# Kernel tuning notes

Measured on AMD Instinct MI355X. Metric: run time of the kernel, lower is better.

Reference implementation:

```python
import jax, jax.numpy as jnp
import numpy as np


def _phi(z, conv_w, conv_b):
    # z: (H, W, S, 1) -> 3x3 SAME conv over state channels -> softmax over states
    x = jnp.transpose(z[..., 0], (2, 0, 1))[None]  # (1, S, H, W)
    y = jax.lax.conv_general_dilated(
        x, conv_w, window_strides=(1, 1), padding='SAME',
        dimension_numbers=('NCHW', 'OIHW', 'NCHW')) + conv_b[None, :, None, None]
    return jax.nn.softmax(jnp.transpose(y[0], (1, 2, 0)), axis=2)[..., None]  # (H, W, S, 1)


def _update(obs, P, u_k, w_k_O, conv_w, conv_b):
    H, W, O = obs.shape
    S = P.shape[0]
    # b = P^T @ obs per cell: b[h,w,s] = sum_o P[o,s] * obs[h,w,o]
    b = jnp.einsum('os,hwo->hws', P, obs)[..., None]  # (H, W, S, 1)
    # Analytic Jacobian db/dP: deriv_b[h,w,s,0,i,j] = obs[h,w,i] * delta(s==j)
    eye = jnp.eye(S, O, dtype=obs.dtype)
    deriv_b = (obs[:, :, None, :, None] * eye[None, None, :, None, :])[:, :, :, None, :, :]  # (H,W,S,1,S,O)

    Bu = b * u_k                                  # (H, W, S, 1)
    bu = jnp.sum(Bu, axis=2, keepdims=True)       # (H, W, 1, 1)
    Z = Bu / bu                                   # Bu / bu

    u_kp1 = _phi(Z, conv_w, conv_b)               # (H, W, S, 1)

    # Sensitivity recursion for obs params (quotient rule on Bu/bu)
    du = deriv_b * u_k[..., None, None] + b[..., None, None] * w_k_O  # (H,W,S,1,S,O)
    term1 = du * bu[..., None, None]
    term2 = jnp.expand_dims(jnp.sum(du, axis=2), 3) * Bu[..., None, None]
    w_pre = (term1 - term2) / bu[..., None, None] ** 2                # (H,W,S,1,S,O)

    # J @ w  ==  9 JVPs of Phi at Z with tangent columns of w (exact, avoids dense (HWS)^2 Jacobian)
    tangents = jnp.moveaxis(w_pre.reshape(H, W, S, 1, S * O), -1, 0)  # (S*O, H, W, S, 1)
    jvp1 = lambda t: jax.jvp(lambda z: _phi(z, conv_w, conv_b), (Z,), (t,))[1]
    w_kp1_O = jnp.moveaxis(jax.vmap(jvp1)(tangents), 0, -1).reshape(H, W, S, 1, S, O)
    return u_kp1, w_kp1_O


def setup_inputs() -> dict:
    key = jax.random.key(0)
    k1, k2, k3 = jax.random.split(key, 3)
    H = W = 512
    S = O = 3
    obs = jax.random.uniform(k1, (H, W, O), dtype=jnp.float32)
    obs_param_matrix = jnp.ones((S, O), jnp.float32) / O          # row-stochastic init
    u_k = jnp.ones((H, W, S, 1), jnp.float32) / S                 # uniform belief
    w_k_O = jnp.zeros((H, W, S, 1, S, O), jnp.float32)
    conv_w = jax.random.normal(k2, (S, S, 3, 3), jnp.float32) * 0.1
    conv_b = jax.random.normal(k3, (S,), jnp.float32) * 0.1
    return {'obs': obs, 'obs_param_matrix': obs_param_matrix, 'u_k': u_k,
            'w_k_O': w_k_O, 'conv_w': conv_w, 'conv_b': conv_b}


def reference(obs, obs_param_matrix, u_k, w_k_O, conv_w, conv_b):
    return _update(obs, obs_param_matrix, u_k, w_k_O, conv_w, conv_b)
```

## Files before the change

kernel.cpp:

```cpp
#include <hip/hip_runtime.h>

#define IMH 512
#define IMW 512
#define TW 16
#define TH 8
#define HW_ (TW + 2)
#define HH_ (TH + 2)
#define NHALO (HW_ * HH_)
#define NPIX (TW * TH)
#define ROW 31

typedef float f4 __attribute__((ext_vector_type(4)));
typedef float f4a __attribute__((ext_vector_type(4), aligned(4)));
typedef float f2a __attribute__((ext_vector_type(2), aligned(4)));

__global__ __launch_bounds__(256, 4)
void hmm_fused(const float* __restrict__ obs,
               const float* __restrict__ P,
               const float* __restrict__ u_k,
               const float* __restrict__ w_k,
               const float* __restrict__ conv_w,
               const float* __restrict__ conv_b,
               float* __restrict__ out) {
    __shared__ __align__(16) float lds[NHALO * ROW];
    __shared__ f4 p_aux4[NPIX];

    const int tid = threadIdx.x;
    const int w0 = blockIdx.x * TW;
    const int h0 = blockIdx.y * TH;

    float Pm[9];
#pragma unroll
    for (int i = 0; i < 9; ++i) Pm[i] = P[i];

    if (tid < NHALO) {
        const int p = tid;
        const int hh = h0 + p / HW_ - 1;
        const int ww = w0 + p % HW_ - 1;
        float* row = &lds[p * ROW];
        if (hh < 0 || hh >= IMH || ww < 0 || ww >= IMW) {
#pragma unroll
            for (int c = 0; c < 30; ++c) row[c] = 0.0f;
        } else {
            const int pix = hh * IMW + ww;

            const f2a o01 = *(const f2a*)(obs + pix * 3);
            const float o2 = obs[pix * 3 + 2];
            const f2a u01 = *(const f2a*)(u_k + pix * 3);
            const float u2 = u_k[pix * 3 + 2];
            const float ov[3] = {o01.x, o01.y, o2};
            const float us[3] = {u01.x, u01.y, u2};

            const float* wkp = &w_k[(size_t)pix * 27];
            float wreg[27];
            {
                const f4a* v4 = (const f4a*)wkp;
                const f4a a0 = v4[0], a1 = v4[1], a2 = v4[2], a3 = v4[3], a4 = v4[4], a5 = v4[5];
                const f2a a6 = *(const f2a*)(wkp + 24);
                const float a7 = wkp[26];
                wreg[0] = a0.x;  wreg[1] = a0.y;  wreg[2] = a0.z;  wreg[3] = a0.w;
                wreg[4] = a1.x;  wreg[5] = a1.y;  wreg[6] = a1.z;  wreg[7] = a1.w;
                wreg[8] = a2.x;  wreg[9] = a2.y;  wreg[10] = a2.z; wreg[11] = a2.w;
                wreg[12] = a3.x; wreg[13] = a3.y; wreg[14] = a3.z; wreg[15] = a3.w;
                wreg[16] = a4.x; wreg[17] = a4.y; wreg[18] = a4.z; wreg[19] = a4.w;
                wreg[20] = a5.x; wreg[21] = a5.y; wreg[22] = a5.z; wreg[23] = a5.w;
                wreg[24] = a6.x; wreg[25] = a6.y; wreg[26] = a7;
            }

            float b[3], Bu[3], bu = 0.0f;
#pragma unroll
            for (int s = 0; s < 3; ++s) {
                b[s] = Pm[0 * 3 + s] * ov[0] + Pm[1 * 3 + s] * ov[1] + Pm[2 * 3 + s] * ov[2];
                Bu[s] = b[s] * us[s];
                bu += Bu[s];
            }
            const float inv_bu = 1.0f / bu;
            float Z[3];
#pragma unroll
            for (int s = 0; s < 3; ++s) { Z[s] = Bu[s] * inv_bu; row[s] = Z[s]; }

#pragma unroll
            for (int i = 0; i < 3; ++i) {
#pragma unroll
                for (int j = 0; j < 3; ++j) {
                    const int ij = i * 3 + j;
                    float du[3], sdu = 0.0f;
#pragma unroll
                    for (int s = 0; s < 3; ++s) {
                        float d = b[s] * wreg[s * 9 + ij];
                        if (s == j) d += ov[i] * us[s];
                        du[s] = d;
                        sdu += d;
                    }
#pragma unroll
                    for (int s = 0; s < 3; ++s)
                        row[(1 + ij) * 3 + s] = (du[s] - sdu * Z[s]) * inv_bu;
                }
            }
        }
    }

    float cw[81];
#pragma unroll
    for (int i = 0; i < 81; ++i) cw[i] = conv_w[i];
    const float cb0 = conv_b[0], cb1 = conv_b[1], cb2 = conv_b[2];

    __syncthreads();

    float* outw = out + IMH * IMW * 3;

    if (tid < NPIX) {
        const int tx = tid & 15, ty = tid >> 4;
        const int hp = (ty + 1) * HW_ + (tx + 1);
        const int pix = (h0 + ty) * IMW + (w0 + tx);
        float y0 = cb0, y1 = cb1, y2 = cb2;
#pragma unroll
        for (int ky = 0; ky < 3; ++ky) {
#pragma unroll
            for (int kx = 0; kx < 3; ++kx) {
                const float* nb = &lds[(hp + (ky - 1) * HW_ + (kx - 1)) * ROW];
                const float v0 = nb[0], v1 = nb[1], v2 = nb[2];
                const int T = ky * 3 + kx;
                y0 += cw[0 + T] * v0 + cw[9 + T] * v1 + cw[18 + T] * v2;
                y1 += cw[27 + T] * v0 + cw[36 + T] * v1 + cw[45 + T] * v2;
                y2 += cw[54 + T] * v0 + cw[63 + T] * v1 + cw[72 + T] * v2;
            }
        }
        const float m = fmaxf(y0, fmaxf(y1, y2));
        const float e0 = __expf(y0 - m), e1 = __expf(y1 - m), e2 = __expf(y2 - m);
        const float inv = 1.0f / (e0 + e1 + e2);
        const float p0 = e0 * inv, p1 = e1 * inv, p2 = e2 * inv;
        out[pix * 3 + 0] = p0; out[pix * 3 + 1] = p1; out[pix * 3 + 2] = p2;
        p_aux4[tid] = (f4){p0, p1, p2, 0.0f};
    }

    __syncthreads();

    if (tid < 144) {
        const int x = tid & 15;
        const int g = (tid >> 4) + 1;
        const int ij = g - 1;
        const int gch = 3 * g;

        float a00, a01, a02;
        float b10, b11, b12;
        float c20, c21, c22;

#define ROWFMA(P0_, P1_, P2_, KY)                                                        \
        P0_ += cw[0 + (KY)*3 + 0] * v00 + cw[9 + (KY)*3 + 0] * v01 + cw[18 + (KY)*3 + 0] * v02; \
        P1_ += cw[27 + (KY)*3 + 0] * v00 + cw[36 + (KY)*3 + 0] * v01 + cw[45 + (KY)*3 + 0] * v02; \
        P2_ += cw[54 + (KY)*3 + 0] * v00 + cw[63 + (KY)*3 + 0] * v01 + cw[72 + (KY)*3 + 0] * v02; \
        P0_ += cw[0 + (KY)*3 + 1] * v10 + cw[9 + (KY)*3 + 1] * v11 + cw[18 + (KY)*3 + 1] * v12; \
        P1_ += cw[27 + (KY)*3 + 1] * v10 + cw[36 + (KY)*3 + 1] * v11 + cw[45 + (KY)*3 + 1] * v12; \
        P2_ += cw[54 + (KY)*3 + 1] * v10 + cw[63 + (KY)*3 + 1] * v11 + cw[72 + (KY)*3 + 1] * v12; \
        P0_ += cw[0 + (KY)*3 + 2] * v20 + cw[9 + (KY)*3 + 2] * v21 + cw[18 + (KY)*3 + 2] * v22; \
        P1_ += cw[27 + (KY)*3 + 2] * v20 + cw[36 + (KY)*3 + 2] * v21 + cw[45 + (KY)*3 + 2] * v22; \
        P2_ += cw[54 + (KY)*3 + 2] * v20 + cw[63 + (KY)*3 + 2] * v21 + cw[72 + (KY)*3 + 2] * v22;

#define FINISH(O, Q0, Q1, Q2) {                                                          \
        const f4 pv = p_aux4[(O) * 16 + x];                                              \
        const float dot_ = pv.x * (Q0) + pv.y * (Q1) + pv.z * (Q2);                      \
        float* wp = outw + ((size_t)((h0 + (O)) * IMW + (w0 + x))) * 27 + ij;            \
        wp[0]  = pv.x * ((Q0) - dot_);                                                   \
        wp[9]  = pv.y * ((Q1) - dot_);                                                   \
        wp[18] = pv.z * ((Q2) - dot_); }

#define STEP(R, N0,N1,N2, M0,M1,M2, O0,O1,O2, DO_N, DO_M, DO_O) {                        \
        const int rb = ((R) * HW_ + x) * ROW + gch;                                      \
        const float v00 = lds[rb + 0],  v01 = lds[rb + 1],  v02 = lds[rb + 2];           \
        const float v10 = lds[rb + 31], v11 = lds[rb + 32], v12 = lds[rb + 33];          \
        const float v20 = lds[rb + 62], v21 = lds[rb + 63], v22 = lds[rb + 64];          \
        if (DO_N) { N0 = 0.0f; N1 = 0.0f; N2 = 0.0f; ROWFMA(N0, N1, N2, 0) }             \
        if (DO_M) { ROWFMA(M0, M1, M2, 1) }                                              \
        if (DO_O) { ROWFMA(O0, O1, O2, 2) FINISH((R) - 2, O0, O1, O2) } }

        STEP(0, a00,a01,a02, b10,b11,b12, c20,c21,c22, true,  false, false)
        STEP(1, b10,b11,b12, a00,a01,a02, c20,c21,c22, true,  true,  false)
        STEP(2, c20,c21,c22, b10,b11,b12, a00,a01,a02, true,  true,  true )
        STEP(3, a00,a01,a02, c20,c21,c22, b10,b11,b12, true,  true,  true )
        STEP(4, b10,b11,b12, a00,a01,a02, c20,c21,c22, true,  true,  true )
        STEP(5, c20,c21,c22, b10,b11,b12, a00,a01,a02, true,  true,  true )
        STEP(6, a00,a01,a02, c20,c21,c22, b10,b11,b12, true,  true,  true )
        STEP(7, b10,b11,b12, a00,a01,a02, c20,c21,c22, true,  true,  true )
        STEP(8, c20,c21,c22, b10,b11,b12, a00,a01,a02, false, true,  true )
        STEP(9, a00,a01,a02, c20,c21,c22, b10,b11,b12, false, false, true )

#undef STEP
#undef FINISH
#undef ROWFMA
    }
}

extern "C" void kernel_launch(void* const* d_in, const int* in_sizes, int n_in,
                              void* d_out, int out_size, void* d_ws, size_t ws_size,
                              hipStream_t stream) {
    const float* obs    = (const float*)d_in[0];
    const float* P      = (const float*)d_in[1];
    const float* u_k    = (const float*)d_in[2];
    const float* w_k    = (const float*)d_in[3];
    const float* conv_w = (const float*)d_in[4];
    const float* conv_b = (const float*)d_in[5];
    float* out = (float*)d_out;

    dim3 grid(IMW / TW, IMH / TH);
    hmm_fused<<<grid, 256, 0, stream>>>(obs, P, u_k, w_k, conv_w, conv_b, out);
}
```

Before: 105.6 us.

## Rebalance JVP work across all threads, split tile rows into halves

The ninth tangent column is moved into the first phase, which already runs one thread per pixel (128 threads). The remaining eight columns are handled by all 256 threads, each covering half the tile rows (4 output rows instead of 8). Previously only 144 threads did the second phase. This removes thread idleness and shortens the serial row loop, at the cost of more halo-row reloads, since each half restarts its sliding window.

Result: no change. 106.8 us (median of 2 runs) (+1.2%).

```diff
diff --git a/kernel.cpp b/kernel.cpp
--- a/kernel.cpp
+++ b/kernel.cpp
@@ -132,15 +132,36 @@
         const float p0 = e0 * inv, p1 = e1 * inv, p2 = e2 * inv;
         out[pix * 3 + 0] = p0; out[pix * 3 + 1] = p1; out[pix * 3 + 2] = p2;
         p_aux4[tid] = (f4){p0, p1, p2, 0.0f};
+
+        float a0 = 0.0f, a1 = 0.0f, a2 = 0.0f;
+#pragma unroll
+        for (int ky = 0; ky < 3; ++ky) {
+#pragma unroll
+            for (int kx = 0; kx < 3; ++kx) {
+                const float* nb = &lds[(hp + (ky - 1) * HW_ + (kx - 1)) * ROW];
+                const float v0 = nb[27], v1 = nb[28], v2 = nb[29];
+                const int T = ky * 3 + kx;
+                a0 += cw[0 + T] * v0 + cw[9 + T] * v1 + cw[18 + T] * v2;
+                a1 += cw[27 + T] * v0 + cw[36 + T] * v1 + cw[45 + T] * v2;
+                a2 += cw[54 + T] * v0 + cw[63 + T] * v1 + cw[72 + T] * v2;
+            }
+        }
+        const float dot_ = p0 * a0 + p1 * a1 + p2 * a2;
+        float* wp = outw + (size_t)pix * 27;
+        wp[8]  = p0 * (a0 - dot_);
+        wp[17] = p1 * (a1 - dot_);
+        wp[26] = p2 * (a2 - dot_);
     }
 
     __syncthreads();
 
-    if (tid < 144) {
+    {
         const int x = tid & 15;
-        const int g = (tid >> 4) + 1;
+        const int g = ((tid >> 4) & 7) + 1;
         const int ij = g - 1;
         const int gch = 3 * g;
+        const int half = tid >> 7;
+        const int rowb = half * 4;
 
         float a00, a01, a02;
         float b10, b11, b12;
@@ -166,24 +187,20 @@
         wp[18] = pv.z * ((Q2) - dot_); }
 
 #define STEP(R, N0,N1,N2, M0,M1,M2, O0,O1,O2, DO_N, DO_M, DO_O) {                        \
-        const int rb = ((R) * HW_ + x) * ROW + gch;                                      \
+        const int rb = ((rowb + (R)) * HW_ + x) * ROW + gch;                             \
         const float v00 = lds[rb + 0],  v01 = lds[rb + 1],  v02 = lds[rb + 2];           \
         const float v10 = lds[rb + 31], v11 = lds[rb + 32], v12 = lds[rb + 33];          \
         const float v20 = lds[rb + 62], v21 = lds[rb + 63], v22 = lds[rb + 64];          \
         if (DO_N) { N0 = 0.0f; N1 = 0.0f; N2 = 0.0f; ROWFMA(N0, N1, N2, 0) }             \
         if (DO_M) { ROWFMA(M0, M1, M2, 1) }                                              \
-        if (DO_O) { ROWFMA(O0, O1, O2, 2) FINISH((R) - 2, O0, O1, O2) } }
+        if (DO_O) { ROWFMA(O0, O1, O2, 2) FINISH(rowb + (R) - 2, O0, O1, O2) } }
 
         STEP(0, a00,a01,a02, b10,b11,b12, c20,c21,c22, true,  false, false)
         STEP(1, b10,b11,b12, a00,a01,a02, c20,c21,c22, true,  true,  false)
         STEP(2, c20,c21,c22, b10,b11,b12, a00,a01,a02, true,  true,  true )
         STEP(3, a00,a01,a02, c20,c21,c22, b10,b11,b12, true,  true,  true )
-        STEP(4, b10,b11,b12, a00,a01,a02, c20,c21,c22, true,  true,  true )
-        STEP(5, c20,c21,c22, b10,b11,b12, a00,a01,a02, true,  true,  true )
-        STEP(6, a00,a01,a02, c20,c21,c22, b10,b11,b12, true,  true,  true )
-        STEP(7, b10,b11,b12, a00,a01,a02, c20,c21,c22, true,  true,  true )
-        STEP(8, c20,c21,c22, b10,b11,b12, a00,a01,a02, false, true,  true )
-        STEP(9, a00,a01,a02, c20,c21,c22, b10,b11,b12, false, false, true )
+        STEP(4, b10,b11,b12, a00,a01,a02, c20,c21,c22, false, true,  true )
+        STEP(5, c20,c21,c22, b10,b11,b12, a00,a01,a02, false, false, true )
 
 #undef STEP
 #undef FINISH
```
